# Optimization experiments

Measured on AMD Instinct MI355X. Metric: run time of the kernel, lower is better.

The kernel has to match this reference:

```python
import jax, jax.numpy as jnp
import numpy as np

B, U, D = 4096, 256, 128  # batch, units (classes), feature dim


def setup_inputs() -> dict:
    key = jax.random.key(0)
    kx, kw, kb = jax.random.split(key, 3)
    # Scale so points lie well inside the unit Poincare ball (c = 1).
    x = jax.random.normal(kx, (B, D), dtype=jnp.float32) * 0.05
    W = jax.random.normal(kw, (U, D), dtype=jnp.float32) * 0.05
    bias = (jax.random.uniform(kb, (U, D), dtype=jnp.float32) * 2.0 - 1.0) * 0.05
    return {"x": x, "W": W, "bias": bias}


def reference(x, W, bias):
    # c = 1 throughout (module hardcodes c = 1.0).
    def sqnorm(t):
        return jnp.sum(t * t, axis=-1, keepdims=True)

    nb2 = sqnorm(bias)                     # [U,1]  ||p_k||^2
    lam = 2.0 / (1.0 - nb2)                # [U,1]  lambda_{p_k}
    # parallel_transport: lambda_x(0)/lambda_x(bias) * W = (1 - ||bias||^2) * W
    a_k = (1.0 - nb2) * W                  # [U,D]
    a_norm = jnp.sqrt(sqnorm(a_k))         # [U,1]

    # mobius_add(-bias, x), broadcast instead of tiling x to [B,U,D]
    u = -bias[None, :, :]                  # [1,U,D]
    v = x[:, None, :]                      # [B,1,D]
    xy = jnp.sum(u * v, axis=-1, keepdims=True)   # [B,U,1]
    nu2 = nb2[None, :, :]                  # [1,U,1]
    nv2 = sqnorm(v)                        # [B,1,1]
    dd = 1.0 + 2.0 * xy + nu2 * nv2
    m = ((1.0 + 2.0 * xy + nv2) * u + (1.0 - nu2) * v) / dd   # [B,U,D]

    num = 2.0 * jnp.sum(m * a_k[None], axis=-1)               # [B,U]
    den = (1.0 - jnp.sum(m * m, axis=-1)) * a_norm[None, :, 0]  # [B,U]
    logits = (lam * a_norm)[None, :, 0] * jnp.arcsinh(num / den)  # [B,U]
    # exp(logits) / sum(exp(logits)) == softmax(logits) (stable form)
    return jax.nn.softmax(logits, axis=-1)
```

## Files before the change

kernel.cpp:

```cpp
#include <hip/hip_runtime.h>
#include <hip/hip_bf16.h>
#include <math.h>

#define BN 4096
#define UN 256
#define DN 128
#define MROW 16
#define BLOCK 1024
#define LSTRIDE 260

typedef __attribute__((ext_vector_type(8))) short short8x;
typedef __attribute__((ext_vector_type(4))) float float4x;

__device__ inline uint pack2bf(float a, float b) {
    __hip_bfloat16 ha = __float2bfloat16(a);
    __hip_bfloat16 hb = __float2bfloat16(b);
    return (uint)(*(ushort*)&ha) | ((uint)(*(ushort*)&hb) << 16);
}

__global__ __launch_bounds__(BLOCK, 4) void fused_kernel(
    const float* __restrict__ x,
    const float* __restrict__ W,
    const float* __restrict__ bias,
    float* __restrict__ out)
{
    __shared__ __align__(16) float logits[MROW][LSTRIDE];

    const int t    = threadIdx.x;
    const int lane = t & 63;
    const int wave = t >> 6;
    const int m16  = lane & 15;
    const int q    = lane >> 4;
    const int b0   = blockIdx.x * MROW;
    const int u    = wave * 16 + m16;

    short8x afrag[4];
    float sq = 0.f;
    {
        const float* xr = x + (size_t)(b0 + m16) * DN + q * 8;
        #pragma unroll
        for (int ks = 0; ks < 4; ++ks) {
            const float4 a = *(const float4*)(xr + ks * 32);
            const float4 b = *(const float4*)(xr + ks * 32 + 4);
            sq = fmaf(a.x, a.x, sq); sq = fmaf(a.y, a.y, sq);
            sq = fmaf(a.z, a.z, sq); sq = fmaf(a.w, a.w, sq);
            sq = fmaf(b.x, b.x, sq); sq = fmaf(b.y, b.y, sq);
            sq = fmaf(b.z, b.z, sq); sq = fmaf(b.w, b.w, sq);
            uint4 p;
            p.x = pack2bf(a.x, a.y);  p.y = pack2bf(a.z, a.w);
            p.z = pack2bf(b.x, b.y);  p.w = pack2bf(b.z, b.w);
            afrag[ks] = *(short8x*)&p;
        }
    }
    sq += __shfl_xor(sq, 16);
    sq += __shfl_xor(sq, 32);

    short8x wfrag[4], bfrag[4];
    float nb2 = 0.f, bw = 0.f, wn2 = 0.f;
    {
        const float* wr = W    + (size_t)u * DN + q * 8;
        const float* br = bias + (size_t)u * DN + q * 8;
        #pragma unroll
        for (int ks = 0; ks < 4; ++ks) {
            const float4 w0 = *(const float4*)(wr + ks * 32);
            const float4 w1 = *(const float4*)(wr + ks * 32 + 4);
            const float4 c0 = *(const float4*)(br + ks * 32);
            const float4 c1 = *(const float4*)(br + ks * 32 + 4);
            nb2 = fmaf(c0.x,c0.x, fmaf(c0.y,c0.y, fmaf(c0.z,c0.z, fmaf(c0.w,c0.w,
                  fmaf(c1.x,c1.x, fmaf(c1.y,c1.y, fmaf(c1.z,c1.z, fmaf(c1.w,c1.w, nb2))))))));
            bw  = fmaf(c0.x,w0.x, fmaf(c0.y,w0.y, fmaf(c0.z,w0.z, fmaf(c0.w,w0.w,
                  fmaf(c1.x,w1.x, fmaf(c1.y,w1.y, fmaf(c1.z,w1.z, fmaf(c1.w,w1.w, bw))))))));
            wn2 = fmaf(w0.x,w0.x, fmaf(w0.y,w0.y, fmaf(w0.z,w0.z, fmaf(w0.w,w0.w,
                  fmaf(w1.x,w1.x, fmaf(w1.y,w1.y, fmaf(w1.z,w1.z, fmaf(w1.w,w1.w, wn2))))))));
            uint4 pw, pb;
            pw.x = pack2bf(w0.x, w0.y);  pw.y = pack2bf(w0.z, w0.w);
            pw.z = pack2bf(w1.x, w1.y);  pw.w = pack2bf(w1.z, w1.w);
            pb.x = pack2bf(c0.x, c0.y);  pb.y = pack2bf(c0.z, c0.w);
            pb.z = pack2bf(c1.x, c1.y);  pb.w = pack2bf(c1.z, c1.w);
            wfrag[ks] = *(short8x*)&pw;
            bfrag[ks] = *(short8x*)&pb;
        }
    }
    nb2 += __shfl_xor(nb2, 16);  nb2 += __shfl_xor(nb2, 32);
    bw  += __shfl_xor(bw , 16);  bw  += __shfl_xor(bw , 32);
    wn2 += __shfl_xor(wn2, 16);  wn2 += __shfl_xor(wn2, 32);

    float4x accW = {0.f, 0.f, 0.f, 0.f};
    float4x accB = {0.f, 0.f, 0.f, 0.f};
    #pragma unroll
    for (int ks = 0; ks < 4; ++ks) {
        accW = __builtin_amdgcn_mfma_f32_16x16x32_bf16(afrag[ks], wfrag[ks], accW, 0, 0, 0);
        accB = __builtin_amdgcn_mfma_f32_16x16x32_bf16(afrag[ks], bfrag[ks], accB, 0, 0, 0);
    }

    const float one_m  = 1.0f - nb2;
    const float a_norm = fabsf(one_m) * sqrtf(wn2);
    const float scale  = (2.0f / one_m) * a_norm;
    #pragma unroll
    for (int rg = 0; rg < 4; ++rg) {
        const int   mr   = q * 4 + rg;
        const float nv2  = __shfl(sq, mr);
        const float dot1 = accW[rg];
        const float xy   = -accB[rg];
        const float dd   = 1.0f + 2.0f * xy + nb2 * nv2;
        const float inv_dd = __builtin_amdgcn_rcpf(dd);
        const float alpha  = (1.0f + 2.0f * xy + nv2) * inv_dd;
        const float beta   = one_m * inv_dd;
        const float num = 2.0f * one_m * (beta * dot1 - alpha * bw);
        const float mm  = alpha * alpha * nb2 + 2.0f * alpha * beta * xy
                        + beta * beta * nv2;
        const float den = (1.0f - mm) * a_norm;
        const float z   = num * __builtin_amdgcn_rcpf(den);
        const float s   = sqrtf(fmaf(z, z, 1.0f));
        logits[mr][u] = scale * copysignf(__logf(fabsf(z) + s), z);
    }
    __syncthreads();

    {
        const int r = wave;
        const float4 v = *(const float4*)&logits[r][lane * 4];
        float mx = fmaxf(fmaxf(v.x, v.y), fmaxf(v.z, v.w));
        #pragma unroll
        for (int off = 32; off; off >>= 1) mx = fmaxf(mx, __shfl_xor(mx, off));
        float4 e;
        e.x = __expf(v.x - mx);  e.y = __expf(v.y - mx);
        e.z = __expf(v.z - mx);  e.w = __expf(v.w - mx);
        float s = e.x + e.y + e.z + e.w;
        #pragma unroll
        for (int off = 32; off; off >>= 1) s += __shfl_xor(s, off);
        const float inv = __builtin_amdgcn_rcpf(s);
        e.x *= inv;  e.y *= inv;  e.z *= inv;  e.w *= inv;
        ((float4*)(out + (size_t)(b0 + r) * UN))[lane] = e;
    }
}

extern "C" void kernel_launch(void* const* d_in, const int* in_sizes, int n_in,
                              void* d_out, int out_size, void* d_ws, size_t ws_size,
                              hipStream_t stream) {
    const float* x    = (const float*)d_in[0];
    const float* W    = (const float*)d_in[1];
    const float* bias = (const float*)d_in[2];
    float* out = (float*)d_out;
    hipLaunchKernelGGL(fused_kernel, dim3(BN / MROW), dim3(BLOCK), 0, stream,
                       x, W, bias, out);
}
```

Measured before the change: 70.49 us.

## Split bf16 packing and norm precompute into prep kernels before main kernel

Adds two prep kernels that convert W, bias and x to bf16 in MFMA fragment order and precompute per-unit norms/scales and per-row squared norms into the workspace. The main kernel then loads pre-swizzled fragments directly, so each of the 256 blocks no longer rereads and repacks the fp32 W and bias. The cost is two extra launches and a round trip through global memory for the packed x.

```diff
diff --git a/kernel.cpp b/kernel.cpp
--- a/kernel.cpp
+++ b/kernel.cpp
@@ -12,94 +12,106 @@
 typedef __attribute__((ext_vector_type(8))) short short8x;
 typedef __attribute__((ext_vector_type(4))) float float4x;
 
+
 __device__ inline uint pack2bf(float a, float b) {
     __hip_bfloat16 ha = __float2bfloat16(a);
     __hip_bfloat16 hb = __float2bfloat16(b);
     return (uint)(*(ushort*)&ha) | ((uint)(*(ushort*)&hb) << 16);
 }
 
-__global__ __launch_bounds__(BLOCK, 4) void fused_kernel(
-    const float* __restrict__ x,
-    const float* __restrict__ W,
-    const float* __restrict__ bias,
-    float* __restrict__ out)
+__global__ __launch_bounds__(64) void prep_wb(
+    const float* __restrict__ W, const float* __restrict__ bias,
+    ushort* __restrict__ Wp, ushort* __restrict__ Bp, float4* __restrict__ S)
 {
-    __shared__ __align__(16) float logits[MROW][LSTRIDE];
+    const int u = blockIdx.x;
+    const int l = threadIdx.x;
+    const float2 w2 = ((const float2*)(W    + (size_t)u * DN))[l];
+    const float2 b2 = ((const float2*)(bias + (size_t)u * DN))[l];
+    float nb2 = b2.x*b2.x + b2.y*b2.y;
+    float bw  = b2.x*w2.x + b2.y*w2.y;
+    float wn2 = w2.x*w2.x + w2.y*w2.y;
+    #pragma unroll
+    for (int off = 32; off; off >>= 1) {
+        nb2 += __shfl_xor(nb2, off);
+        bw  += __shfl_xor(bw , off);
+        wn2 += __shfl_xor(wn2, off);
+    }
+    const int d  = 2 * l;
+    const int ks = d >> 5, q = (d & 31) >> 3, j = d & 7;
+    const int chunk = ((u >> 4) * 256) + ks * 64 + q * 16 + (u & 15);
+    ((uint*)Wp)[chunk * 4 + (j >> 1)] = pack2bf(w2.x, w2.y);
+    ((uint*)Bp)[chunk * 4 + (j >> 1)] = pack2bf(b2.x, b2.y);
+    if (l == 0) {
+        const float one_m  = 1.0f - nb2;
+        const float a_norm = fabsf(one_m) * sqrtf(wn2);
+        const float scale  = (2.0f / one_m) * a_norm;
+        S[u] = make_float4(nb2, bw, a_norm, scale);
+    }
+}
+
+__global__ __launch_bounds__(256) void prep_x(
+    const float* __restrict__ x, ushort* __restrict__ Xp, float* __restrict__ NV2)
+{
+    const int tile = blockIdx.x;
+    const int h  = threadIdx.x;
+    const int r  = h >> 4;
+    const int hc = h & 15;
+    const float4* xp4 = (const float4*)(x + (size_t)(tile * MROW + r) * DN + hc * 8);
+    const float4 a = xp4[0], b = xp4[1];
+    float sq = a.x*a.x + a.y*a.y + a.z*a.z + a.w*a.w
+             + b.x*b.x + b.y*b.y + b.z*b.z + b.w*b.w;
+    uint4 p;
+    p.x = pack2bf(a.x, a.y);  p.y = pack2bf(a.z, a.w);
+    p.z = pack2bf(b.x, b.y);  p.w = pack2bf(b.z, b.w);
+    const int ks = hc >> 2, q = hc & 3;
+    ((uint4*)Xp)[tile * 256 + ks * 64 + q * 16 + r] = p;
+    #pragma unroll
+    for (int off = 1; off < 16; off <<= 1) sq += __shfl_xor(sq, off);
+    if (hc == 0) NV2[tile * MROW + r] = sq;
+}
+
+__global__ __launch_bounds__(BLOCK, 4) void main_kernel(
+    const ushort* __restrict__ Xp, const ushort* __restrict__ Wp,
+    const ushort* __restrict__ Bp, const float4* __restrict__ S,
+    const float* __restrict__ NV2, float* __restrict__ out)
+{
+    __shared__ float logits[MROW][LSTRIDE];
 
     const int t    = threadIdx.x;
     const int lane = t & 63;
     const int wave = t >> 6;
     const int m16  = lane & 15;
     const int q    = lane >> 4;
-    const int b0   = blockIdx.x * MROW;
+    const int blk  = blockIdx.x;
+    const int b0   = blk * MROW;
     const int u    = wave * 16 + m16;
 
-    short8x afrag[4];
-    float sq = 0.f;
-    {
-        const float* xr = x + (size_t)(b0 + m16) * DN + q * 8;
-        #pragma unroll
-        for (int ks = 0; ks < 4; ++ks) {
-            const float4 a = *(const float4*)(xr + ks * 32);
-            const float4 b = *(const float4*)(xr + ks * 32 + 4);
-            sq = fmaf(a.x, a.x, sq); sq = fmaf(a.y, a.y, sq);
-            sq = fmaf(a.z, a.z, sq); sq = fmaf(a.w, a.w, sq);
-            sq = fmaf(b.x, b.x, sq); sq = fmaf(b.y, b.y, sq);
-            sq = fmaf(b.z, b.z, sq); sq = fmaf(b.w, b.w, sq);
-            uint4 p;
-            p.x = pack2bf(a.x, a.y);  p.y = pack2bf(a.z, a.w);
-            p.z = pack2bf(b.x, b.y);  p.w = pack2bf(b.z, b.w);
-            afrag[ks] = *(short8x*)&p;
-        }
+    const short8x* xc = (const short8x*)Xp + blk  * 256 + lane;
+    const short8x* wc = (const short8x*)Wp + wave * 256 + lane;
+    const short8x* bc = (const short8x*)Bp + wave * 256 + lane;
+    short8x af[4], wf[4], bf[4];
+    #pragma unroll
+    for (int ks = 0; ks < 4; ++ks) {
+        af[ks] = xc[ks * 64];
+        wf[ks] = wc[ks * 64];
+        bf[ks] = bc[ks * 64];
     }
-    sq += __shfl_xor(sq, 16);
-    sq += __shfl_xor(sq, 32);
-
-    short8x wfrag[4], bfrag[4];
-    float nb2 = 0.f, bw = 0.f, wn2 = 0.f;
-    {
-        const float* wr = W    + (size_t)u * DN + q * 8;
-        const float* br = bias + (size_t)u * DN + q * 8;
-        #pragma unroll
-        for (int ks = 0; ks < 4; ++ks) {
-            const float4 w0 = *(const float4*)(wr + ks * 32);
-            const float4 w1 = *(const float4*)(wr + ks * 32 + 4);
-            const float4 c0 = *(const float4*)(br + ks * 32);
-            const float4 c1 = *(const float4*)(br + ks * 32 + 4);
-            nb2 = fmaf(c0.x,c0.x, fmaf(c0.y,c0.y, fmaf(c0.z,c0.z, fmaf(c0.w,c0.w,
-                  fmaf(c1.x,c1.x, fmaf(c1.y,c1.y, fmaf(c1.z,c1.z, fmaf(c1.w,c1.w, nb2))))))));
-            bw  = fmaf(c0.x,w0.x, fmaf(c0.y,w0.y, fmaf(c0.z,w0.z, fmaf(c0.w,w0.w,
-                  fmaf(c1.x,w1.x, fmaf(c1.y,w1.y, fmaf(c1.z,w1.z, fmaf(c1.w,w1.w, bw))))))));
-            wn2 = fmaf(w0.x,w0.x, fmaf(w0.y,w0.y, fmaf(w0.z,w0.z, fmaf(w0.w,w0.w,
-                  fmaf(w1.x,w1.x, fmaf(w1.y,w1.y, fmaf(w1.z,w1.z, fmaf(w1.w,w1.w, wn2))))))));
-            uint4 pw, pb;
-            pw.x = pack2bf(w0.x, w0.y);  pw.y = pack2bf(w0.z, w0.w);
-            pw.z = pack2bf(w1.x, w1.y);  pw.w = pack2bf(w1.z, w1.w);
-            pb.x = pack2bf(c0.x, c0.y);  pb.y = pack2bf(c0.z, c0.w);
-            pb.z = pack2bf(c1.x, c1.y);  pb.w = pack2bf(c1.z, c1.w);
-            wfrag[ks] = *(short8x*)&pw;
-            bfrag[ks] = *(short8x*)&pb;
-        }
-    }
-    nb2 += __shfl_xor(nb2, 16);  nb2 += __shfl_xor(nb2, 32);
-    bw  += __shfl_xor(bw , 16);  bw  += __shfl_xor(bw , 32);
-    wn2 += __shfl_xor(wn2, 16);  wn2 += __shfl_xor(wn2, 32);
+    const float4 sc  = S[u];
+    const float4 nv4 = ((const float4*)(NV2 + b0))[q];
 
     float4x accW = {0.f, 0.f, 0.f, 0.f};
     float4x accB = {0.f, 0.f, 0.f, 0.f};
     #pragma unroll
     for (int ks = 0; ks < 4; ++ks) {
-        accW = __builtin_amdgcn_mfma_f32_16x16x32_bf16(afrag[ks], wfrag[ks], accW, 0, 0, 0);
-        accB = __builtin_amdgcn_mfma_f32_16x16x32_bf16(afrag[ks], bfrag[ks], accB, 0, 0, 0);
+        accW = __builtin_amdgcn_mfma_f32_16x16x32_bf16(af[ks], wf[ks], accW, 0, 0, 0);
+        accB = __builtin_amdgcn_mfma_f32_16x16x32_bf16(af[ks], bf[ks], accB, 0, 0, 0);
     }
 
-    const float one_m  = 1.0f - nb2;
-    const float a_norm = fabsf(one_m) * sqrtf(wn2);
-    const float scale  = (2.0f / one_m) * a_norm;
+    const float nb2 = sc.x, bw = sc.y, a_norm = sc.z, scale = sc.w;
+    const float one_m = 1.0f - nb2;
     #pragma unroll
     for (int rg = 0; rg < 4; ++rg) {
-        const int   mr   = q * 4 + rg;
-        const float nv2  = __shfl(sq, mr);
+        const float nv2  = ((const float*)&nv4)[rg];
         const float dot1 = accW[rg];
         const float xy   = -accB[rg];
         const float dd   = 1.0f + 2.0f * xy + nb2 * nv2;
@@ -112,7 +124,7 @@
         const float den = (1.0f - mm) * a_norm;
         const float z   = num * __builtin_amdgcn_rcpf(den);
         const float s   = sqrtf(fmaf(z, z, 1.0f));
-        logits[mr][u] = scale * copysignf(__logf(fabsf(z) + s), z);
+        logits[q * 4 + rg][u] = scale * copysignf(__logf(fabsf(z) + s), z);
     }
     __syncthreads();
 
@@ -141,6 +153,16 @@
     const float* W    = (const float*)d_in[1];
     const float* bias = (const float*)d_in[2];
     float* out = (float*)d_out;
-    hipLaunchKernelGGL(fused_kernel, dim3(BN / MROW), dim3(BLOCK), 0, stream,
-                       x, W, bias, out);
+
+    char* ws = (char*)d_ws;
+    ushort* Wp  = (ushort*)(ws);
+    ushort* Bp  = (ushort*)(ws + 65536);
+    float4* S   = (float4*)(ws + 131072);
+    ushort* Xp  = (ushort*)(ws + 135168);
+    float*  NV2 = (float*) (ws + 1183744);
+
+    hipLaunchKernelGGL(prep_wb, dim3(UN), dim3(64), 0, stream, W, bias, Wp, Bp, S);
+    hipLaunchKernelGGL(prep_x, dim3(BN / MROW), dim3(256), 0, stream, x, Xp, NV2);
+    hipLaunchKernelGGL(main_kernel, dim3(BN / MROW), dim3(BLOCK), 0, stream,
+                       Xp, Wp, Bp, S, NV2, out);
 }
```

After: 65.71 us. 6.8% less time.
